# Kernel tuning notes

Measured on AMD Instinct MI355X. Metric: run time of the kernel, lower is better.

## Reference

```python
import jax, jax.numpy as jnp
import numpy as np

N, E, G = 50000, 800000, 512          # nodes, edges, graphs in batch
DIN, DH, H, DOUT = 128, 128, 2, 128   # dim_in, dim_h, heads, dim_out
NEG_SLOPE = 0.2
EPS_BN = 1e-5


def setup_inputs():
    key = jax.random.key(0)
    ks = jax.random.split(key, 12)
    def glorot(k, shape, fan):
        return (jax.random.normal(k, shape, jnp.float32) / np.float32(np.sqrt(fan)))
    return dict(
        x=jax.random.normal(ks[0], (N, DIN), jnp.float32),
        edge_index=jax.random.randint(ks[1], (2, E), 0, N, dtype=jnp.int32),
        batch=jnp.sort(jax.random.randint(ks[2], (N,), 0, G, dtype=jnp.int32)),
        Wl1=glorot(ks[3], (DIN, H * DH), DIN),
        Wr1=glorot(ks[4], (DIN, H * DH), DIN),
        att1=glorot(ks[5], (H, DH), DH),
        b1=jnp.zeros((H * DH,), jnp.float32),
        gamma=jnp.ones((H * DH,), jnp.float32),
        beta=jnp.zeros((H * DH,), jnp.float32),
        Wl2=glorot(ks[6], (H * DH, DOUT), H * DH),
        Wr2=glorot(ks[7], (H * DH, DOUT), H * DH),
        att2=glorot(ks[8], (1, DOUT), DOUT),
        b2=jnp.zeros((DOUT,), jnp.float32),
        Wlin=glorot(ks[9], (DOUT, 2), DOUT),
        blin=jnp.zeros((2,), jnp.float32),
    )


def gatv2_conv(x, src, dst, Wl, Wr, att, bias, heads, dh, n):
    # x: [n, F]; src/dst: [Etot] (self-loops already appended)
    xl = (x @ Wl).reshape(n, heads, dh)  # source transform (messages)
    xr = (x @ Wr).reshape(n, heads, dh)  # target transform
    m = xl[src] + xr[dst]                             # [Etot, H, dh]
    e = jnp.einsum('ehd,hd->eh', jax.nn.leaky_relu(m, NEG_SLOPE), att)  # [Etot, H]
    # softmax over incoming edges of each target node
    emax = jax.ops.segment_max(e, dst, num_segments=n)
    ex = jnp.exp(e - emax[dst])
    denom = jax.ops.segment_sum(ex, dst, num_segments=n)
    alpha = ex / (denom[dst] + 1e-16)                 # [Etot, H]
    out = jax.ops.segment_sum(xl[src] * alpha[:, :, None], dst, num_segments=n)
    return out.reshape(n, heads * dh) + bias


def reference(x, edge_index, batch, Wl1, Wr1, att1, b1, gamma, beta,
              Wl2, Wr2, att2, b2, Wlin, blin):
    loops = jnp.arange(N, dtype=edge_index.dtype)
    src = jnp.concatenate([edge_index[0], loops])
    dst = jnp.concatenate([edge_index[1], loops])

    h = gatv2_conv(x, src, dst, Wl1, Wr1, att1, b1, H, DH, N)   # [N, H*DH]
    h = jax.nn.elu(h)
    # BatchNorm over node dimension (training-mode batch stats)
    mu = h.mean(axis=0)
    var = h.var(axis=0)
    h = (h - mu) * jax.lax.rsqrt(var + EPS_BN) * gamma + beta
    # dropout p=0 -> identity
    h = gatv2_conv(h, src, dst, Wl2, Wr2, att2, b2, 1, DOUT, N)  # [N, DOUT]

    # global mean pool per graph
    s = jax.ops.segment_sum(h, batch, num_segments=G)
    cnt = jax.ops.segment_sum(jnp.ones((N,), h.dtype), batch, num_segments=G)
    pooled = s / jnp.maximum(cnt, 1.0)[:, None]                  # [G, DOUT]
    return pooled @ Wlin + blin                                  # [G, 2]
```

## Files before the change

### kernel.cpp

```cpp
#include <hip/hip_runtime.h>


#define DIN 128
#define F1 256
#define F2 128
#define NEG_SLOPE 0.2f

typedef unsigned short u16;
typedef __attribute__((ext_vector_type(8))) short short8;
typedef __attribute__((ext_vector_type(4))) float floatx4;

__device__ __forceinline__ float bf2f(u16 u) {
  return __uint_as_float(((unsigned int)u) << 16);
}
__device__ __forceinline__ u16 f2bf(float f) {
  unsigned int x = __float_as_uint(f);
  return (u16)((x + 0x7fffu + ((x >> 16) & 1u)) >> 16);
}
__device__ __forceinline__ void load8(const u16* p, float (&f)[8]) {
  short8 v = *(const short8*)p;
#pragma unroll
  for (int k = 0; k < 8; k++) f[k] = bf2f((u16)v[k]);
}

struct PTab { const void* src[8]; int off[9]; };
__global__ __launch_bounds__(256) void k_convert_all(
    const void* __restrict__ xsrc, u16* __restrict__ xb, int n4, int nxb,
    PTab t, u16* __restrict__ pb, int ptotal, int npb,
    const void* __restrict__ Wl1s, const void* __restrict__ Wr1s,
    const void* __restrict__ Wl2s, const void* __restrict__ Wr2s,
    u16* __restrict__ Wl1t, u16* __restrict__ Wr1t,
    u16* __restrict__ Wl2t, u16* __restrict__ Wr2t,
    int* __restrict__ zbase, int zn, int* __restrict__ flag) {
  __shared__ int flagS;
  int tid = threadIdx.x;
  if (tid < 64) {
    int cnt = 0;
#pragma unroll
    for (int i = 0; i < 2; ++i) {
      u16 v = ((const u16*)xsrc)[2 * (tid + 64 * i)];
      int e = (v >> 7) & 0xFF;
      if (e >= 115 && e <= 130) cnt++;
    }
#pragma unroll
    for (int m = 1; m <= 32; m <<= 1) cnt += __shfl_xor(cnt, m, 64);
    if (tid == 0) flagS = (cnt < 64) ? 1 : 0;
  }
  __syncthreads();
  const int fl = flagS;
  if (blockIdx.x == 0 && tid == 0) *flag = fl;

  int b = blockIdx.x;
  if (b < nxb) {
    int i = b * 256 + tid;
    if (i >= n4) return;
    if (fl) {
      float4 a = ((const float4*)xsrc)[i];
      ushort4 o;
      o.x = f2bf(a.x); o.y = f2bf(a.y); o.z = f2bf(a.z); o.w = f2bf(a.w);
      ((ushort4*)xb)[i] = o;
    } else {
      ((ulong1*)xb)[i] = ((const ulong1*)xsrc)[i];
    }
    return;
  }
  b -= nxb;
  if (b < npb) {
    int i = b * 256 + tid;
    if (i >= ptotal) return;
    int s = 0;
#pragma unroll
    for (int k = 1; k < 8; k++) s += (i >= t.off[k]);
    int local = i - t.off[s];
    pb[i] = fl ? f2bf(((const float*)t.src[s])[local]) : ((const u16*)t.src[s])[local];
    return;
  }
  b -= npb;
  if (b < 512) {
    int seg = b >> 7;
    int i = (b & 127) * 256 + tid;
    const void* s; u16* d; int NL, sh;
    if      (seg == 0) { s = Wl1s; d = Wl1t; NL = 256; sh = 7; }
    else if (seg == 1) { s = Wr1s; d = Wr1t; NL = 256; sh = 7; }
    else if (seg == 2) { s = Wl2s; d = Wl2t; NL = 128; sh = 8; }
    else               { s = Wr2s; d = Wr2t; NL = 128; sh = 8; }
    int n = i >> sh, k = i & ((1 << sh) - 1);
    int si = k * NL + n;
    d[i] = fl ? f2bf(((const float*)s)[si]) : ((const u16*)s)[si];
    return;
  }
  b -= 512;
  int i = b * 256 + tid;
  if (i < zn) zbase[i] = 0;
}

__global__ void k_hist(const int* __restrict__ ei, int* __restrict__ hist,
                       int E, int Etot) {
  int e = blockIdx.x * 256 + threadIdx.x;
  if (e >= Etot) return;
  int dst = (e < E) ? ei[E + e] : (e - E);
  atomicAdd(&hist[dst], 1);
}

__global__ void k_scan(const int* __restrict__ hist, int* __restrict__ rowptr,
                       int* __restrict__ cursor, unsigned long long* __restrict__ pstate,
                       int* __restrict__ ctr, int n, int Etot) {
  __shared__ int tmp[256];
  __shared__ int bidS, offS;
  int t = threadIdx.x;
  if (t == 0) bidS = atomicAdd(ctr, 1);
  __syncthreads();
  int bid = bidS;
  int gid = bid * 256 + t;
  int v = (gid < n) ? hist[gid] : 0;
  tmp[t] = v;
  __syncthreads();
  for (int off = 1; off < 256; off <<= 1) {
    int add = (t >= off) ? tmp[t - off] : 0;
    __syncthreads();
    tmp[t] += add;
    __syncthreads();
  }
  if (t == 0) {
    int total = tmp[255];
    unsigned long long st =
        ((unsigned long long)(bid == 0 ? 2 : 1) << 32) | (unsigned)total;
    atomicExch(&pstate[bid], st);
    int off = 0;
    if (bid > 0) {
      int b = bid - 1;
      while (true) {
        unsigned long long s;
        do { s = atomicAdd(&pstate[b], 0ULL); } while ((s >> 32) == 0);
        off += (int)(unsigned)s;
        if ((s >> 32) == 2) break;
        b--;
      }
      atomicExch(&pstate[bid],
                 ((unsigned long long)2 << 32) | (unsigned)(off + total));
    }
    offS = off;
  }
  __syncthreads();
  int off = offS;
  if (gid < n) {
    int ex = off + tmp[t] - v;
    rowptr[gid] = ex;
    cursor[gid] = ex;
  }
  if (gid == 0) rowptr[n] = Etot;
}

__global__ void k_scatter(const int* __restrict__ ei, int* __restrict__ cursor,
                          int* __restrict__ ssrc, int E, int Etot) {
  int e = blockIdx.x * 256 + threadIdx.x;
  if (e >= Etot) return;
  int src, dst;
  if (e < E) { src = ei[e]; dst = ei[E + e]; }
  else       { src = e - E; dst = e - E; }
  int pos = atomicAdd(&cursor[dst], 1);
  ssrc[pos] = src;
}

template<int K, bool RB>
__global__ __launch_bounds__(256) void k_gemm(
    const u16* __restrict__ A, const u16* __restrict__ Blt, const u16* __restrict__ Brt,
    int NL, u16* __restrict__ Cl, u16* __restrict__ Cr, int M,
    const float* __restrict__ rbias) {
  const int tid = threadIdx.x;
  const int m0 = blockIdx.x * 64;
  const int n0g = blockIdx.y * 64;
  const u16* Bt; u16* C; int col0;
  if (n0g < NL) { Bt = Blt; C = Cl; col0 = n0g; }
  else          { Bt = Brt; C = Cr; col0 = n0g - NL; }

  const int wave = tid >> 6, lane = tid & 63;
  const int wm = wave >> 1, wn = wave & 1;
  const int quad = lane >> 4, l16 = lane & 15;

  floatx4 acc[2][2] = {};
#pragma unroll
  for (int k0 = 0; k0 < K; k0 += 32) {
    short8 af[2], bfr[2];
#pragma unroll
    for (int mt = 0; mt < 2; mt++) {
      int row = m0 + wm * 32 + mt * 16 + l16;
      if (row > M - 1) row = M - 1;
      af[mt] = *(const short8*)(A + (size_t)row * K + k0 + quad * 8);
    }
#pragma unroll
    for (int nt = 0; nt < 2; nt++) {
      int nn = col0 + wn * 32 + nt * 16 + l16;
      bfr[nt] = *(const short8*)(Bt + (size_t)nn * K + k0 + quad * 8);
    }
#pragma unroll
    for (int mt = 0; mt < 2; mt++)
#pragma unroll
      for (int nt = 0; nt < 2; nt++)
        acc[mt][nt] = __builtin_amdgcn_mfma_f32_16x16x32_bf16(af[mt], bfr[nt], acc[mt][nt], 0, 0, 0);
  }

#pragma unroll
  for (int mt = 0; mt < 2; mt++)
#pragma unroll
    for (int nt = 0; nt < 2; nt++) {
      float rb = 0.f;
      if (RB) rb = rbias[n0g + wn * 32 + nt * 16 + l16];
#pragma unroll
      for (int r = 0; r < 4; r++) {
        int row = m0 + wm * 32 + mt * 16 + quad * 4 + r;
        if (row < M) {
          int col = col0 + wn * 32 + nt * 16 + l16;
          C[(size_t)row * NL + col] = f2bf(acc[mt][nt][r] + rb);
        }
      }
    }
}

template<int HEADS, int MODE>
__global__ __launch_bounds__(256) void k_agg(
    const u16* __restrict__ xl, const u16* __restrict__ xr,
    const u16* __restrict__ att, const u16* __restrict__ bias,
    const int* __restrict__ rowptr, const int* __restrict__ ssrc,
    void* __restrict__ outv, int n) {
  constexpr int F = HEADS * 128;
  constexpr int EPI = 4 / HEADS;
  int wave = threadIdx.x >> 6, lane = threadIdx.x & 63;
  int node = blockIdx.x * 4 + wave;
  if (node >= n) return;
  const int q = lane >> 4, l = lane & 15;
  const int eo   = (HEADS == 2) ? (q >> 1) : q;
  const int head = (HEADS == 2) ? (q & 1) : 0;
  const int ch0 = head * 128 + l * 8;

  float xrv[8], attv[8], acc[8];
  load8(xr + (size_t)node * F + ch0, xrv);
  load8(att + ch0, attv);
#pragma unroll
  for (int k = 0; k < 8; k++) acc[k] = 0.f;

  float l_run = 0.f;
  const int jb = rowptr[node], je = rowptr[node + 1];
  for (int j = jb; j < je; j += EPI) {
    int jj = j + eo;
    int src = ssrc[jj < je ? jj : (je - 1)];
    float xlv[8];
    load8(xl + (size_t)src * F + ch0, xlv);
    float s = 0.f;
#pragma unroll
    for (int k = 0; k < 8; k++) {
      float mm = xlv[k] + xrv[k];
      mm = mm > 0.f ? mm : NEG_SLOPE * mm;
      s += mm * attv[k];
    }
#pragma unroll
    for (int m = 1; m <= 8; m <<= 1) s += __shfl_xor(s, m, 64);
    float p = (jj < je) ? __expf(fminf(s, 80.f)) : 0.f;
    l_run += p;
#pragma unroll
    for (int k = 0; k < 8; k++) acc[k] += p * xlv[k];
  }

#pragma unroll
  for (int m = 16 * HEADS; m <= 32; m <<= 1) {
#pragma unroll
    for (int k = 0; k < 8; k++) acc[k] += __shfl_xor(acc[k], m, 64);
    l_run += __shfl_xor(l_run, m, 64);
  }

  if (lane < 16 * HEADS) {
    float inv = 1.f / (l_run + 1e-16f);
    if (MODE == 0) {
      short8 o;
#pragma unroll
      for (int k = 0; k < 8; k++) {
        float t = acc[k] * inv + bf2f(bias[ch0 + k]);
        t = t > 0.f ? t : (__expf(t) - 1.f);
        o[k] = (short)f2bf(t);
      }
      *(short8*)((u16*)outv + (size_t)node * F + ch0) = o;
    } else {
      float v[8];
#pragma unroll
      for (int k = 0; k < 8; k++) v[k] = acc[k] * inv + bf2f(bias[ch0 + k]);
      float* op = (float*)outv + (size_t)node * F + ch0;
      *(float4*)op = make_float4(v[0], v[1], v[2], v[3]);
      *(float4*)(op + 4) = make_float4(v[4], v[5], v[6], v[7]);
    }
  }
}

__global__ __launch_bounds__(256) void k_stats(
    const u16* __restrict__ h, float* __restrict__ gsum,
    float* __restrict__ gsumsq, int n) {
  __shared__ float smS[8][256], smQ[8][256];
  int t = threadIdx.x;
  int rg = t >> 5, cl = t & 31;
  int ch0 = cl * 8;
  float s[8] = {}, q[8] = {};
  for (int r = blockIdx.x * 8 + rg; r < n; r += gridDim.x * 8) {
    float v[8];
    load8(h + (size_t)r * F1 + ch0, v);
#pragma unroll
    for (int k = 0; k < 8; k++) { s[k] += v[k]; q[k] += v[k] * v[k]; }
  }
#pragma unroll
  for (int k = 0; k < 8; k++) { smS[rg][ch0 + k] = s[k]; smQ[rg][ch0 + k] = q[k]; }
  __syncthreads();
  float ts = 0.f, tq = 0.f;
#pragma unroll
  for (int g = 0; g < 8; g++) { ts += smS[g][t]; tq += smQ[g][t]; }
  atomicAdd(&gsum[t], ts);
  atomicAdd(&gsumsq[t], tq);
}

__global__ __launch_bounds__(256) void k_foldbn(
    const float* __restrict__ gsum, const float* __restrict__ gsumsq,
    const u16* __restrict__ gamma, const u16* __restrict__ beta,
    u16* __restrict__ Wl2t, u16* __restrict__ Wr2t,
    float* __restrict__ rbias, float invn) {
  __shared__ float red[8];
  int t = threadIdx.x, n = blockIdx.x;
  float mu = gsum[t] * invn;
  float var = gsumsq[t] * invn - mu * mu;
  float a = bf2f(gamma[t]) * rsqrtf(fmaxf(var, 0.f) + 1e-5f);
  float b = bf2f(beta[t]) - mu * a;
  float wl = bf2f(Wl2t[n * 256 + t]);
  float wr = bf2f(Wr2t[n * 256 + t]);
  float sl = b * wl, sr = b * wr;
  Wl2t[n * 256 + t] = f2bf(a * wl);
  Wr2t[n * 256 + t] = f2bf(a * wr);
#pragma unroll
  for (int m = 1; m <= 32; m <<= 1) {
    sl += __shfl_xor(sl, m, 64);
    sr += __shfl_xor(sr, m, 64);
  }
  int wave = t >> 6, lane = t & 63;
  if (lane == 0) { red[wave] = sl; red[4 + wave] = sr; }
  __syncthreads();
  if (t == 0) rbias[n] = red[0] + red[1] + red[2] + red[3];
  if (t == 1) rbias[128 + n] = red[4] + red[5] + red[6] + red[7];
}

__device__ __forceinline__ int lowerb(const int* __restrict__ a, int n, int key) {
  int lo = 0, hi = n;
  while (lo < hi) { int m = (lo + hi) >> 1; if (a[m] < key) lo = m + 1; else hi = m; }
  return lo;
}

__global__ __launch_bounds__(256) void k_poolfinal(
    const float* __restrict__ h2, const int* __restrict__ batch,
    const u16* __restrict__ Wlin, const u16* __restrict__ blin,
    void* __restrict__ out, const int* __restrict__ flag, int G, int N) {
  __shared__ float sm[4][128];
  int g = blockIdx.x;
  int wave = threadIdx.x >> 6, lane = threadIdx.x & 63;
  int jb = lowerb(batch, N, g);
  int je = lowerb(batch, N, g + 1);
  int ch = lane * 2;
  float c0 = 0.f, c1 = 0.f;
  for (int r = jb + wave; r < je; r += 4) {
    float2 v = *(const float2*)(h2 + (size_t)r * F2 + ch);
    c0 += v.x; c1 += v.y;
  }
  sm[wave][ch] = c0;
  sm[wave][ch + 1] = c1;
  __syncthreads();
  if (wave == 0) {
    c0 = sm[0][ch] + sm[1][ch] + sm[2][ch] + sm[3][ch];
    c1 = sm[0][ch + 1] + sm[1][ch + 1] + sm[2][ch + 1] + sm[3][ch + 1];
    float cf = fmaxf((float)(je - jb), 1.f);
    c0 /= cf; c1 /= cf;
    float s0 = c0 * bf2f(Wlin[ch * 2 + 0]) + c1 * bf2f(Wlin[(ch + 1) * 2 + 0]);
    float s1 = c0 * bf2f(Wlin[ch * 2 + 1]) + c1 * bf2f(Wlin[(ch + 1) * 2 + 1]);
#pragma unroll
    for (int m = 1; m <= 32; m <<= 1) {
      s0 += __shfl_xor(s0, m, 64);
      s1 += __shfl_xor(s1, m, 64);
    }
    if (lane == 0) {
      float o0 = s0 + bf2f(blin[0]);
      float o1 = s1 + bf2f(blin[1]);
      if (*flag) {
        ((float*)out)[g * 2 + 0] = o0;
        ((float*)out)[g * 2 + 1] = o1;
      } else {
        ((u16*)out)[g * 2 + 0] = f2bf(o0);
        ((u16*)out)[g * 2 + 1] = f2bf(o1);
      }
    }
  }
}

extern "C" void kernel_launch(void* const* d_in, const int* in_sizes, int n_in,
                              void* d_out, int out_size, void* d_ws, size_t ws_size,
                              hipStream_t stream) {
  const int* ei    = (const int*)d_in[1];
  const int* batch = (const int*)d_in[2];

  const int N = in_sizes[0] / DIN;
  const int E = in_sizes[1] / 2;
  const int G = out_size / 2;
  const int Etot = E + N;

  char* p = (char*)d_ws;
  auto alloc = [&](size_t bytes) {
    char* r = p;
    p += (bytes + 255) & ~(size_t)255;
    return r;
  };
  int*  flag     = (int*)alloc(256);
  int*  hist     = (int*)alloc((size_t)N * 4);
  float* gsum    = (float*)alloc(1024);
  float* gsumsq  = (float*)alloc(1024);
  unsigned long long* pstate = (unsigned long long*)alloc(2048);
  int*  ctr      = (int*)alloc(256);
  int   zn       = (int)(((char*)ctr + 256) - (char*)hist) / 4;
  int*  rowptr   = (int*)alloc((size_t)(N + 1) * 4);
  int*  cursor   = (int*)alloc((size_t)N * 4);
  float* rbias   = (float*)alloc(256 * 4);
  int*  ssrc     = (int*)alloc((size_t)Etot * 4);
  u16*  xb       = (u16*)alloc((size_t)N * DIN * 2);
  u16*  pb       = (u16*)alloc(4096);
  u16*  Wl1t     = (u16*)alloc(DIN * F1 * 2);
  u16*  Wr1t     = (u16*)alloc(DIN * F1 * 2);
  u16*  Wl2t     = (u16*)alloc(F1 * F2 * 2);
  u16*  Wr2t     = (u16*)alloc(F1 * F2 * 2);
  u16*  regionA  = (u16*)alloc((size_t)N * F1 * 2);
  u16*  regionB  = (u16*)alloc((size_t)N * F1 * 2);
  u16*  regionC  = (u16*)alloc((size_t)N * F1 * 2);

  u16*  xl1  = regionA;
  u16*  xr1  = regionB;
  u16*  helu = regionC;
  u16*  xl2  = regionB;
  u16*  xr2  = regionB + (size_t)N * F2;
  float* h2  = (float*)regionA;

  const int pidx[8] = {5, 6, 7, 8, 11, 12, 13, 14};
  PTab tab;
  int accum = 0;
  for (int i = 0; i < 8; i++) {
    tab.src[i] = d_in[pidx[i]];
    tab.off[i] = accum;
    accum += in_sizes[pidx[i]];
  }
  tab.off[8] = accum;
  int n4 = in_sizes[0] / 4;
  int nxb = (n4 + 255) / 256;
  int npb = (accum + 255) / 256;
  int nzb = (zn + 255) / 256;
  k_convert_all<<<nxb + npb + 512 + nzb, 256, 0, stream>>>(
      d_in[0], xb, n4, nxb, tab, pb, accum, npb,
      d_in[3], d_in[4], d_in[9], d_in[10], Wl1t, Wr1t, Wl2t, Wr2t,
      hist, zn, flag);
  u16 *pAtt1 = pb + tab.off[0], *pB1 = pb + tab.off[1], *pGamma = pb + tab.off[2],
      *pBeta = pb + tab.off[3], *pAtt2 = pb + tab.off[4], *pB2 = pb + tab.off[5],
      *pWlin = pb + tab.off[6], *pBlin = pb + tab.off[7];

  const int eb = (Etot + 255) / 256;
  const int sb = (N + 255) / 256;

  k_hist<<<eb, 256, 0, stream>>>(ei, hist, E, Etot);
  k_scan<<<sb, 256, 0, stream>>>(hist, rowptr, cursor, pstate, ctr, N, Etot);
  k_scatter<<<eb, 256, 0, stream>>>(ei, cursor, ssrc, E, Etot);

  dim3 g1((N + 63) / 64, (2 * F1) / 64);
  k_gemm<DIN, false><<<g1, 256, 0, stream>>>(xb, Wl1t, Wr1t, F1, xl1, xr1, N, nullptr);

  k_agg<2, 0><<<(N + 3) / 4, 256, 0, stream>>>(xl1, xr1, pAtt1, pB1, rowptr, ssrc, helu, N);

  k_stats<<<256, 256, 0, stream>>>(helu, gsum, gsumsq, N);
  k_foldbn<<<128, 256, 0, stream>>>(gsum, gsumsq, pGamma, pBeta, Wl2t, Wr2t, rbias,
                                    1.0f / (float)N);

  dim3 g2((N + 63) / 64, (2 * F2) / 64);
  k_gemm<F1, true><<<g2, 256, 0, stream>>>(helu, Wl2t, Wr2t, F2, xl2, xr2, N, rbias);

  k_agg<1, 1><<<(N + 3) / 4, 256, 0, stream>>>(xl2, xr2, pAtt2, pB2, rowptr, ssrc, h2, N);

  k_poolfinal<<<G, 256, 0, stream>>>(h2, batch, pWlin, pBlin, d_out, flag, G, N);
}
```

Before: 455.2 us.

## Fuse histogram with first GEMM, fold BN finalize into stats and GEMM2 load

Merges the edge-histogram kernel with the first projection GEMM into one launch so the two independent jobs share a grid. The BN-stats kernel now finalizes the scale and shift in its last block, using an atomic counter. It also writes bias-only outputs for empty graphs, which the pool kernel now skips. The second GEMM applies the BN affine to activations as it loads them, instead of folding it into the weights, which removes the fold kernel and two launches. The cost is extra per-element conversion arithmetic inside the GEMM2 K loop, plus a grid-wide atomic-counter handoff.

```diff
diff --git a/kernel.cpp b/kernel.cpp
--- a/kernel.cpp
+++ b/kernel.cpp
@@ -94,12 +94,78 @@
   if (i < zn) zbase[i] = 0;
 }
 
-__global__ void k_hist(const int* __restrict__ ei, int* __restrict__ hist,
-                       int E, int Etot) {
-  int e = blockIdx.x * 256 + threadIdx.x;
-  if (e >= Etot) return;
-  int dst = (e < E) ? ei[E + e] : (e - E);
-  atomicAdd(&hist[dst], 1);
+template<int K, bool RB>
+__device__ __forceinline__ void gemm_body(
+    const u16* __restrict__ A, const u16* __restrict__ Blt, const u16* __restrict__ Brt,
+    int NL, u16* __restrict__ Cl, u16* __restrict__ Cr, int M,
+    const float* __restrict__ rbias, int bx, int by, int tid) {
+  const int m0 = bx * 64;
+  const int n0g = by * 64;
+  const u16* Bt; u16* C; int col0;
+  if (n0g < NL) { Bt = Blt; C = Cl; col0 = n0g; }
+  else          { Bt = Brt; C = Cr; col0 = n0g - NL; }
+
+  const int wave = tid >> 6, lane = tid & 63;
+  const int wm = wave >> 1, wn = wave & 1;
+  const int quad = lane >> 4, l16 = lane & 15;
+
+  floatx4 acc[2][2] = {};
+#pragma unroll
+  for (int k0 = 0; k0 < K; k0 += 32) {
+    short8 af[2], bfr[2];
+#pragma unroll
+    for (int mt = 0; mt < 2; mt++) {
+      int row = m0 + wm * 32 + mt * 16 + l16;
+      if (row > M - 1) row = M - 1;
+      af[mt] = *(const short8*)(A + (size_t)row * K + k0 + quad * 8);
+    }
+#pragma unroll
+    for (int nt = 0; nt < 2; nt++) {
+      int nn = col0 + wn * 32 + nt * 16 + l16;
+      bfr[nt] = *(const short8*)(Bt + (size_t)nn * K + k0 + quad * 8);
+    }
+#pragma unroll
+    for (int mt = 0; mt < 2; mt++)
+#pragma unroll
+      for (int nt = 0; nt < 2; nt++)
+        acc[mt][nt] = __builtin_amdgcn_mfma_f32_16x16x32_bf16(af[mt], bfr[nt], acc[mt][nt], 0, 0, 0);
+  }
+
+#pragma unroll
+  for (int mt = 0; mt < 2; mt++)
+#pragma unroll
+    for (int nt = 0; nt < 2; nt++) {
+      float rb = 0.f;
+      if (RB) rb = rbias[n0g + wn * 32 + nt * 16 + l16];
+#pragma unroll
+      for (int r = 0; r < 4; r++) {
+        int row = m0 + wm * 32 + mt * 16 + quad * 4 + r;
+        if (row < M) {
+          int col = col0 + wn * 32 + nt * 16 + l16;
+          C[(size_t)row * NL + col] = f2bf(acc[mt][nt][r] + rb);
+        }
+      }
+    }
+}
+
+__global__ __launch_bounds__(256) void k_histgemm1(
+    const int* __restrict__ ei, int* __restrict__ hist,
+    const int* __restrict__ batch, int* __restrict__ gcnt, int E, int Etot, int N,
+    int eb, const u16* __restrict__ xb, const u16* __restrict__ Wl1t,
+    const u16* __restrict__ Wr1t, u16* __restrict__ xl1, u16* __restrict__ xr1,
+    int Mt) {
+  int b = blockIdx.x;
+  if (b < eb) {
+    int e = b * 256 + threadIdx.x;
+    if (e >= Etot) return;
+    int dst = (e < E) ? ei[E + e] : (e - E);
+    atomicAdd(&hist[dst], 1);
+    if (e < N) atomicAdd(&gcnt[batch[e]], 1);
+    return;
+  }
+  b -= eb;
+  gemm_body<DIN, false>(xb, Wl1t, Wr1t, F1, xl1, xr1, N, nullptr, b % Mt, b / Mt,
+                        threadIdx.x);
 }
 
 __global__ void k_scan(const int* __restrict__ hist, int* __restrict__ rowptr,
@@ -160,61 +226,6 @@
   else       { src = e - E; dst = e - E; }
   int pos = atomicAdd(&cursor[dst], 1);
   ssrc[pos] = src;
-}
-
-template<int K, bool RB>
-__global__ __launch_bounds__(256) void k_gemm(
-    const u16* __restrict__ A, const u16* __restrict__ Blt, const u16* __restrict__ Brt,
-    int NL, u16* __restrict__ Cl, u16* __restrict__ Cr, int M,
-    const float* __restrict__ rbias) {
-  const int tid = threadIdx.x;
-  const int m0 = blockIdx.x * 64;
-  const int n0g = blockIdx.y * 64;
-  const u16* Bt; u16* C; int col0;
-  if (n0g < NL) { Bt = Blt; C = Cl; col0 = n0g; }
-  else          { Bt = Brt; C = Cr; col0 = n0g - NL; }
-
-  const int wave = tid >> 6, lane = tid & 63;
-  const int wm = wave >> 1, wn = wave & 1;
-  const int quad = lane >> 4, l16 = lane & 15;
-
-  floatx4 acc[2][2] = {};
-#pragma unroll
-  for (int k0 = 0; k0 < K; k0 += 32) {
-    short8 af[2], bfr[2];
-#pragma unroll
-    for (int mt = 0; mt < 2; mt++) {
-      int row = m0 + wm * 32 + mt * 16 + l16;
-      if (row > M - 1) row = M - 1;
-      af[mt] = *(const short8*)(A + (size_t)row * K + k0 + quad * 8);
-    }
-#pragma unroll
-    for (int nt = 0; nt < 2; nt++) {
-      int nn = col0 + wn * 32 + nt * 16 + l16;
-      bfr[nt] = *(const short8*)(Bt + (size_t)nn * K + k0 + quad * 8);
-    }
-#pragma unroll
-    for (int mt = 0; mt < 2; mt++)
-#pragma unroll
-      for (int nt = 0; nt < 2; nt++)
-        acc[mt][nt] = __builtin_amdgcn_mfma_f32_16x16x32_bf16(af[mt], bfr[nt], acc[mt][nt], 0, 0, 0);
-  }
-
-#pragma unroll
-  for (int mt = 0; mt < 2; mt++)
-#pragma unroll
-    for (int nt = 0; nt < 2; nt++) {
-      float rb = 0.f;
-      if (RB) rb = rbias[n0g + wn * 32 + nt * 16 + l16];
-#pragma unroll
-      for (int r = 0; r < 4; r++) {
-        int row = m0 + wm * 32 + mt * 16 + quad * 4 + r;
-        if (row < M) {
-          int col = col0 + wn * 32 + nt * 16 + l16;
-          C[(size_t)row * NL + col] = f2bf(acc[mt][nt][r] + rb);
-        }
-      }
-    }
 }
 
 template<int HEADS, int MODE>
@@ -290,15 +301,19 @@
   }
 }
 
-__global__ __launch_bounds__(256) void k_stats(
-    const u16* __restrict__ h, float* __restrict__ gsum,
-    float* __restrict__ gsumsq, int n) {
+__global__ __launch_bounds__(256) void k_stats2(
+    const u16* __restrict__ h, float* __restrict__ gsum, float* __restrict__ gsumsq,
+    const u16* __restrict__ gamma, const u16* __restrict__ beta,
+    float* __restrict__ ab, const int* __restrict__ gcnt,
+    const u16* __restrict__ blin, const int* __restrict__ flag,
+    void* __restrict__ out, int* __restrict__ sctr, int n, int G, float invn) {
   __shared__ float smS[8][256], smQ[8][256];
+  __shared__ int lastS;
   int t = threadIdx.x;
   int rg = t >> 5, cl = t & 31;
   int ch0 = cl * 8;
   float s[8] = {}, q[8] = {};
-  for (int r = blockIdx.x * 8 + rg; r < n; r += gridDim.x * 8) {
+  for (int r = blockIdx.x * 8 + rg; r < n; r += 256 * 8) {
     float v[8];
     load8(h + (size_t)r * F1 + ch0, v);
 #pragma unroll
@@ -312,34 +327,93 @@
   for (int g = 0; g < 8; g++) { ts += smS[g][t]; tq += smQ[g][t]; }
   atomicAdd(&gsum[t], ts);
   atomicAdd(&gsumsq[t], tq);
-}
-
-__global__ __launch_bounds__(256) void k_foldbn(
-    const float* __restrict__ gsum, const float* __restrict__ gsumsq,
-    const u16* __restrict__ gamma, const u16* __restrict__ beta,
-    u16* __restrict__ Wl2t, u16* __restrict__ Wr2t,
-    float* __restrict__ rbias, float invn) {
-  __shared__ float red[8];
-  int t = threadIdx.x, n = blockIdx.x;
-  float mu = gsum[t] * invn;
-  float var = gsumsq[t] * invn - mu * mu;
-  float a = bf2f(gamma[t]) * rsqrtf(fmaxf(var, 0.f) + 1e-5f);
-  float b = bf2f(beta[t]) - mu * a;
-  float wl = bf2f(Wl2t[n * 256 + t]);
-  float wr = bf2f(Wr2t[n * 256 + t]);
-  float sl = b * wl, sr = b * wr;
-  Wl2t[n * 256 + t] = f2bf(a * wl);
-  Wr2t[n * 256 + t] = f2bf(a * wr);
-#pragma unroll
-  for (int m = 1; m <= 32; m <<= 1) {
-    sl += __shfl_xor(sl, m, 64);
-    sr += __shfl_xor(sr, m, 64);
-  }
-  int wave = t >> 6, lane = t & 63;
-  if (lane == 0) { red[wave] = sl; red[4 + wave] = sr; }
-  __syncthreads();
-  if (t == 0) rbias[n] = red[0] + red[1] + red[2] + red[3];
-  if (t == 1) rbias[128 + n] = red[4] + red[5] + red[6] + red[7];
+
+  __threadfence();
+  __syncthreads();
+  if (t == 0) lastS = (atomicAdd(sctr, 1) == 255) ? 1 : 0;
+  __syncthreads();
+  if (lastS) {
+    __threadfence();
+    float gs = atomicAdd(&gsum[t], 0.f);
+    float gq = atomicAdd(&gsumsq[t], 0.f);
+    float mu = gs * invn;
+    float var = gq * invn - mu * mu;
+    float a = bf2f(gamma[t]) * rsqrtf(fmaxf(var, 0.f) + 1e-5f);
+    ab[t] = a;
+    ab[256 + t] = bf2f(beta[t]) - mu * a;
+    for (int g = t; g < G; g += 256) {
+      if (gcnt[g] == 0) {
+        float o0 = bf2f(blin[0]), o1 = bf2f(blin[1]);
+        if (*flag) {
+          ((float*)out)[g * 2 + 0] = o0;
+          ((float*)out)[g * 2 + 1] = o1;
+        } else {
+          ((u16*)out)[g * 2 + 0] = f2bf(o0);
+          ((u16*)out)[g * 2 + 1] = f2bf(o1);
+        }
+      }
+    }
+  }
+}
+
+__global__ __launch_bounds__(256) void k_gemm2bn(
+    const u16* __restrict__ A, const u16* __restrict__ Blt, const u16* __restrict__ Brt,
+    u16* __restrict__ Cl, u16* __restrict__ Cr, int M, const float* __restrict__ ab) {
+  const int tid = threadIdx.x;
+  const int m0 = blockIdx.x * 64;
+  const int n0g = blockIdx.y * 64;
+  const u16* Bt; u16* C; int col0;
+  if (n0g < F2) { Bt = Blt; C = Cl; col0 = n0g; }
+  else          { Bt = Brt; C = Cr; col0 = n0g - F2; }
+
+  const int wave = tid >> 6, lane = tid & 63;
+  const int wm = wave >> 1, wn = wave & 1;
+  const int quad = lane >> 4, l16 = lane & 15;
+
+  floatx4 acc[2][2] = {};
+#pragma unroll
+  for (int k0 = 0; k0 < F1; k0 += 32) {
+    float av[8], bv[8];
+    *(float4*)av       = *(const float4*)(ab + k0 + quad * 8);
+    *(float4*)(av + 4) = *(const float4*)(ab + k0 + quad * 8 + 4);
+    *(float4*)bv       = *(const float4*)(ab + 256 + k0 + quad * 8);
+    *(float4*)(bv + 4) = *(const float4*)(ab + 256 + k0 + quad * 8 + 4);
+    short8 af[2], bfr[2];
+#pragma unroll
+    for (int mt = 0; mt < 2; mt++) {
+      int row = m0 + wm * 32 + mt * 16 + l16;
+      if (row > M - 1) row = M - 1;
+      short8 raw = *(const short8*)(A + (size_t)row * F1 + k0 + quad * 8);
+#pragma unroll
+      for (int j = 0; j < 8; j++) {
+        float v = av[j] * bf2f((u16)raw[j]) + bv[j];
+        af[mt][j] = (short)f2bf(v);
+      }
+    }
+#pragma unroll
+    for (int nt = 0; nt < 2; nt++) {
+      int nn = col0 + wn * 32 + nt * 16 + l16;
+      bfr[nt] = *(const short8*)(Bt + (size_t)nn * F1 + k0 + quad * 8);
+    }
+#pragma unroll
+    for (int mt = 0; mt < 2; mt++)
+#pragma unroll
+      for (int nt = 0; nt < 2; nt++)
+        acc[mt][nt] = __builtin_amdgcn_mfma_f32_16x16x32_bf16(af[mt], bfr[nt], acc[mt][nt], 0, 0, 0);
+  }
+
+#pragma unroll
+  for (int mt = 0; mt < 2; mt++)
+#pragma unroll
+    for (int nt = 0; nt < 2; nt++)
+#pragma unroll
+      for (int r = 0; r < 4; r++) {
+        int row = m0 + wm * 32 + mt * 16 + quad * 4 + r;
+        if (row < M) {
+          int col = col0 + wn * 32 + nt * 16 + l16;
+          C[(size_t)row * F2 + col] = f2bf(acc[mt][nt][r]);
+        }
+      }
 }
 
 __device__ __forceinline__ int lowerb(const int* __restrict__ a, int n, int key) {
@@ -357,6 +431,7 @@
   int wave = threadIdx.x >> 6, lane = threadIdx.x & 63;
   int jb = lowerb(batch, N, g);
   int je = lowerb(batch, N, g + 1);
+  if (jb >= je) return;
   int ch = lane * 2;
   float c0 = 0.f, c1 = 0.f;
   for (int r = jb + wave; r < je; r += 4) {
@@ -415,10 +490,12 @@
   float* gsumsq  = (float*)alloc(1024);
   unsigned long long* pstate = (unsigned long long*)alloc(2048);
   int*  ctr      = (int*)alloc(256);
-  int   zn       = (int)(((char*)ctr + 256) - (char*)hist) / 4;
+  int*  gcnt     = (int*)alloc((size_t)G * 4);
+  int*  sctr     = (int*)alloc(256);
+  int   zn       = (int)(((char*)sctr + 256) - (char*)hist) / 4;
   int*  rowptr   = (int*)alloc((size_t)(N + 1) * 4);
   int*  cursor   = (int*)alloc((size_t)N * 4);
-  float* rbias   = (float*)alloc(256 * 4);
+  float* ab      = (float*)alloc(2048);
   int*  ssrc     = (int*)alloc((size_t)Etot * 4);
   u16*  xb       = (u16*)alloc((size_t)N * DIN * 2);
   u16*  pb       = (u16*)alloc(4096);
@@ -460,22 +537,19 @@
 
   const int eb = (Etot + 255) / 256;
   const int sb = (N + 255) / 256;
-
-  k_hist<<<eb, 256, 0, stream>>>(ei, hist, E, Etot);
+  const int Mt = (N + 63) / 64;
+
+  k_histgemm1<<<eb + Mt * 8, 256, 0, stream>>>(ei, hist, batch, gcnt, E, Etot, N,
+                                               eb, xb, Wl1t, Wr1t, xl1, xr1, Mt);
   k_scan<<<sb, 256, 0, stream>>>(hist, rowptr, cursor, pstate, ctr, N, Etot);
   k_scatter<<<eb, 256, 0, stream>>>(ei, cursor, ssrc, E, Etot);
 
-  dim3 g1((N + 63) / 64, (2 * F1) / 64);
-  k_gemm<DIN, false><<<g1, 256, 0, stream>>>(xb, Wl1t, Wr1t, F1, xl1, xr1, N, nullptr);
-
   k_agg<2, 0><<<(N + 3) / 4, 256, 0, stream>>>(xl1, xr1, pAtt1, pB1, rowptr, ssrc, helu, N);
 
-  k_stats<<<256, 256, 0, stream>>>(helu, gsum, gsumsq, N);
-  k_foldbn<<<128, 256, 0, stream>>>(gsum, gsumsq, pGamma, pBeta, Wl2t, Wr2t, rbias,
-                                    1.0f / (float)N);
-
-  dim3 g2((N + 63) / 64, (2 * F2) / 64);
-  k_gemm<F1, true><<<g2, 256, 0, stream>>>(helu, Wl2t, Wr2t, F2, xl2, xr2, N, rbias);
+  k_stats2<<<256, 256, 0, stream>>>(helu, gsum, gsumsq, pGamma, pBeta, ab, gcnt,
+                                    pBlin, flag, d_out, sctr, N, G, 1.0f / (float)N);
+
+  k_gemm2bn<<<dim3(Mt, 4), 256, 0, stream>>>(helu, Wl2t, Wr2t, xl2, xr2, N, ab);
 
   k_agg<1, 1><<<(N + 3) / 4, 256, 0, stream>>>(xl2, xr2, pAtt2, pB2, rowptr, ssrc, h2, N);
 
```

Result: slower. 508.7 us (+11.8%).
